# Performance work log

Hardware: AMD Instinct MI355X
Metric: run time of the kernel (lower is better)

The kernel has to match this reference:

```python
import jax, jax.numpy as jnp
import numpy as np

N = 1_000_000
H, W = 480, 640
MIN_DEPTH, MAX_DEPTH = 0.0, 30.0


def setup_inputs() -> dict:
    key = jax.random.key(0)
    k1, k2, k3 = jax.random.split(key, 3)
    scale = jnp.array([W - 1, H - 1], dtype=jnp.float32)
    mkpts0_f = jax.random.uniform(k1, (N, 2), dtype=jnp.float32) * scale
    mkpts1_f = jax.random.uniform(k2, (N, 2), dtype=jnp.float32) * scale
    mconf = jax.random.uniform(k3, (N,), dtype=jnp.float32)
    K = jnp.array([[520.0, 0.0, 320.0],
                   [0.0, 520.0, 240.0],
                   [0.0, 0.0, 1.0]], dtype=jnp.float32)
    K0 = K[None]  # [1,3,3]
    K1 = K[None]
    c, s = float(np.cos(0.1)), float(np.sin(0.1))
    T_0to1 = jnp.array([[c, 0.0, s, 0.2],
                        [0.0, 1.0, 0.0, 0.0],
                        [-s, 0.0, c, 0.05],
                        [0.0, 0.0, 0.0, 1.0]], dtype=jnp.float32)[None]  # [1,4,4]
    image0 = jnp.zeros((1, 1, H, W), dtype=jnp.float32)
    m_bids = jnp.zeros((N,), dtype=jnp.int32)  # single batch element
    return {"T_0to1": T_0to1, "K0": K0, "K1": K1, "mconf": mconf,
            "mkpts0_f": mkpts0_f, "mkpts1_f": mkpts1_f,
            "image0": image0, "m_bids": m_bids}


def _triangulate(T_0to1, K0, K1, mconf, kpts0, kpts1):
    # Projection matrices: P0 = K0 @ [I|0], P1 = K1 @ T[:3,:]
    proj_identity = jnp.eye(3, 4, dtype=K0.dtype)
    P0 = K0[0] @ proj_identity          # [3,4]
    P1 = K1[0] @ T_0to1[0, :3, :]       # [3,4]
    P = jnp.stack([P0, P1], axis=0)     # [V=2,3,4]

    pts = jnp.stack([kpts0, kpts1], axis=1)              # [N,2,2]
    conf = jnp.stack([jnp.ones_like(mconf), mconf], 1)   # [N,2] (self conf = 1)

    # A[n,v] = pts[n,v,:,None] * P[v,2,None,:] - P[v,:2]   -> [N,V,2,4]
    A = pts[..., None] * P[None, :, 2, None, :] - P[None, :, :2, :]
    A = A * conf[:, :, None, None]
    A = A.reshape(A.shape[0], 4, 4)                       # [N,4,4]

    # torch.svd returns V with A = U S V^T; jnp gives Vh = V^T.
    _, _, Vh = jnp.linalg.svd(A)
    v = -Vh[:, 3, :]                                      # [N,4] = -V[:,:,3]
    points_3d = v[:, :3] / v[:, 3:4]                      # homogeneous -> euclidean
    # torch clamps to [-1000,1000] only when infs appear; the final depth value
    # after [0,30] clamp + filter is identical either way, so clip unconditionally.
    points_3d = jnp.clip(points_3d, -1000.0, 1000.0)

    z = jnp.clip(points_3d[:, 2], MIN_DEPTH, MAX_DEPTH)
    filt = (z > MIN_DEPTH) & (z < MAX_DEPTH)
    kp3d_val = z * filt.astype(z.dtype)
    return kp3d_val, points_3d


def reference(T_0to1, K0, K1, mconf, mkpts0_f, mkpts1_f, image0, m_bids):
    h, w = image0.shape[-2], image0.shape[-1]
    kp3d_val, _ = _triangulate(T_0to1, K0, K1, mconf, mkpts0_f, mkpts1_f)
    # generate_sparse_depth: depth[0, y, x] = kp3d_val (long() truncation)
    xi = mkpts0_f[:, 0].astype(jnp.int32)
    yi = mkpts0_f[:, 1].astype(jnp.int32)
    depth0_sparse = jnp.zeros((1, h, w), dtype=kp3d_val.dtype).at[0, yi, xi].set(kp3d_val)
    return depth0_sparse, kp3d_val
```

## Files before the change

kernel.cpp:

```cpp
#include <hip/hip_runtime.h>
#include <math.h>

#define N_PTS 1000000
#define H_IMG 480
#define W_IMG 640
#define PIX (H_IMG * W_IMG)
#define TPB 256
#define BPTS 1024
#define NBLK ((N_PTS + BPTS - 1) / BPTS)


#define ROT64(p, q)                                                            \
  do {                                                                         \
    double apq = Mv[p][q];                                                     \
    if (apq != 0.0) {                                                          \
      double app = Mv[p][p], aqq = Mv[q][q];                                   \
      double d = aqq - app;                                                    \
      double r = sqrt(fma(d, d, 4.0 * apq * apq));                             \
      double t = (2.0 * apq) / (d + copysign(r, d));                           \
      double c = rsqrt(fma(t, t, 1.0));                                        \
      double s = t * c;                                                        \
      Mv[p][p] = fma(-t, apq, app);                                            \
      Mv[q][q] = fma(t, apq, aqq);                                             \
      Mv[p][q] = 0.0;                                                          \
      Mv[q][p] = 0.0;                                                          \
      _Pragma("unroll") for (int k = 0; k < 4; k++) {                          \
        if (k != p && k != q) {                                                \
          double akp = Mv[k][p], akq = Mv[k][q];                               \
          double nkp = c * akp - s * akq;                                      \
          double nkq = s * akp + c * akq;                                      \
          Mv[k][p] = nkp; Mv[p][k] = nkp;                                      \
          Mv[k][q] = nkq; Mv[q][k] = nkq;                                      \
        }                                                                      \
      }                                                                        \
      { double v2p = Vr2[p], v2q = Vr2[q];                                     \
        Vr2[p] = c * v2p - s * v2q; Vr2[q] = s * v2p + c * v2q; }              \
      { double v3p = Vr3[p], v3q = Vr3[q];                                     \
        Vr3[p] = c * v3p - s * v3q; Vr3[q] = s * v3p + c * v3q; }              \
    }                                                                          \
  } while (0)

__device__ float tri_point_fp64(int n,
                                const float* __restrict__ T,
                                const float* __restrict__ K0,
                                const float* __restrict__ K1,
                                const float* __restrict__ mconf,
                                const float* __restrict__ kp0,
                                const float* __restrict__ kp1) {
  float2 p0 = ((const float2*)kp0)[n];
  float2 p1 = ((const float2*)kp1)[n];
  double conf = (double)mconf[n];
  double x0 = (double)p0.x, y0 = (double)p0.y;
  double x1 = (double)p1.x, y1 = (double)p1.y;

  double P0[3][4];
#pragma unroll
  for (int i = 0; i < 3; i++) {
#pragma unroll
    for (int j = 0; j < 3; j++) P0[i][j] = (double)K0[i * 3 + j];
    P0[i][3] = 0.0;
  }
  double P1[3][4];
#pragma unroll
  for (int i = 0; i < 3; i++) {
#pragma unroll
    for (int j = 0; j < 4; j++) {
      double s = 0.0;
#pragma unroll
      for (int k = 0; k < 3; k++)
        s += (double)K1[i * 3 + k] * (double)T[k * 4 + j];
      P1[i][j] = s;
    }
  }

  double Mv[4][4];
#pragma unroll
  for (int i = 0; i < 4; i++)
#pragma unroll
    for (int j = 0; j < 4; j++) Mv[i][j] = 0.0;

  double a[4];
#pragma unroll
  for (int j = 0; j < 4; j++) a[j] = x0 * P0[2][j] - P0[0][j];
#pragma unroll
  for (int i = 0; i < 4; i++)
#pragma unroll
    for (int j = 0; j < 4; j++) Mv[i][j] = fma(a[i], a[j], Mv[i][j]);
#pragma unroll
  for (int j = 0; j < 4; j++) a[j] = y0 * P0[2][j] - P0[1][j];
#pragma unroll
  for (int i = 0; i < 4; i++)
#pragma unroll
    for (int j = 0; j < 4; j++) Mv[i][j] = fma(a[i], a[j], Mv[i][j]);
#pragma unroll
  for (int j = 0; j < 4; j++) a[j] = conf * (x1 * P1[2][j] - P1[0][j]);
#pragma unroll
  for (int i = 0; i < 4; i++)
#pragma unroll
    for (int j = 0; j < 4; j++) Mv[i][j] = fma(a[i], a[j], Mv[i][j]);
#pragma unroll
  for (int j = 0; j < 4; j++) a[j] = conf * (y1 * P1[2][j] - P1[1][j]);
#pragma unroll
  for (int i = 0; i < 4; i++)
#pragma unroll
    for (int j = 0; j < 4; j++) Mv[i][j] = fma(a[i], a[j], Mv[i][j]);

  double Vr2[4] = {0.0, 0.0, 1.0, 0.0};
  double Vr3[4] = {0.0, 0.0, 0.0, 1.0};

  for (int sweep = 0; sweep < 4; sweep++) {
    ROT64(0, 1); ROT64(0, 2); ROT64(0, 3);
    ROT64(1, 2); ROT64(1, 3); ROT64(2, 3);
  }

  double e0 = Mv[0][0], e1 = Mv[1][1], e2 = Mv[2][2], e3 = Mv[3][3];
  bool b01 = e1 < e0;
  double ea = b01 ? e1 : e0;
  double za = b01 ? Vr2[1] : Vr2[0];
  double wa = b01 ? Vr3[1] : Vr3[0];
  bool b23 = e3 < e2;
  double eb = b23 ? e3 : e2;
  double zb = b23 ? Vr2[3] : Vr2[2];
  double wb = b23 ? Vr3[3] : Vr3[2];
  bool bf = eb < ea;
  double vz = bf ? zb : za;
  double vw = bf ? wb : wa;

  double z = vz / vw;
  z = fmin(fmax(z, 0.0), 30.0);
  bool filt = (z > 0.0) && (z < 30.0);
  return filt ? (float)z : 0.0f;
}

#define ROTF(p, q)                                                             \
  do {                                                                         \
    float apq = Mv[p][q];                                                      \
    if (apq != 0.0f) {                                                         \
      float app = Mv[p][p], aqq = Mv[q][q];                                    \
      float d = aqq - app;                                                     \
      float r = sqrtf(fmaf(d, d, 4.0f * apq * apq));                           \
      float t = __fdividef(2.0f * apq, d + copysignf(r, d));                   \
      float c = rsqrtf(fmaf(t, t, 1.0f));                                      \
      float s = t * c;                                                         \
      Mv[p][p] = fmaf(-t, apq, app);                                           \
      Mv[q][q] = fmaf(t, apq, aqq);                                            \
      Mv[p][q] = 0.0f;                                                         \
      Mv[q][p] = 0.0f;                                                         \
      _Pragma("unroll") for (int k = 0; k < 4; k++) {                          \
        if (k != p && k != q) {                                                \
          float akp = Mv[k][p], akq = Mv[k][q];                                \
          float nkp = c * akp - s * akq;                                       \
          float nkq = s * akp + c * akq;                                       \
          Mv[k][p] = nkp; Mv[p][k] = nkp;                                      \
          Mv[k][q] = nkq; Mv[q][k] = nkq;                                      \
        }                                                                      \
      }                                                                        \
      { float v2p = Vr2[p], v2q = Vr2[q];                                      \
        Vr2[p] = c * v2p - s * v2q; Vr2[q] = s * v2p + c * v2q; }              \
      { float v3p = Vr3[p], v3q = Vr3[q];                                      \
        Vr3[p] = c * v3p - s * v3q; Vr3[q] = s * v3p + c * v3q; }              \
    }                                                                          \
  } while (0)

__global__ __launch_bounds__(TPB) void tri_main(
    const float* __restrict__ T,
    const float* __restrict__ K0,
    const float* __restrict__ K1,
    const float* __restrict__ mconf,
    const float* __restrict__ kp0,
    const float* __restrict__ kp1,
    float* __restrict__ out_kp3d,
    unsigned long long* __restrict__ ws_pix)
{
  __shared__ unsigned short s_list[BPTS];
  __shared__ int s_cnt;

  int tid = threadIdx.x;
  int base = blockIdx.x * BPTS;
  if (tid == 0) s_cnt = 0;
  __syncthreads();

  float P0[3][4];
#pragma unroll
  for (int i = 0; i < 3; i++) {
#pragma unroll
    for (int j = 0; j < 3; j++) P0[i][j] = K0[i * 3 + j];
    P0[i][3] = 0.0f;
  }
  float P1[3][4];
#pragma unroll
  for (int i = 0; i < 3; i++) {
#pragma unroll
    for (int j = 0; j < 4; j++) {
      float s = 0.0f;
#pragma unroll
      for (int k = 0; k < 3; k++) s += K1[i * 3 + k] * T[k * 4 + j];
      P1[i][j] = s;
    }
  }

#pragma unroll 1
  for (int r = 0; r < BPTS / TPB; r++) {
    int local = r * TPB + tid;
    int n = base + local;
    if (n >= N_PTS) break;

    float2 p0 = ((const float2*)kp0)[n];
    float2 p1 = ((const float2*)kp1)[n];
    float conf = mconf[n];
    float x0 = p0.x, y0 = p0.y, x1 = p1.x, y1 = p1.y;

    float Mv[4][4];
#pragma unroll
    for (int i = 0; i < 4; i++)
#pragma unroll
      for (int j = 0; j < 4; j++) Mv[i][j] = 0.0f;

    float a[4];
#pragma unroll
    for (int j = 0; j < 4; j++) a[j] = x0 * P0[2][j] - P0[0][j];
#pragma unroll
    for (int i = 0; i < 4; i++)
#pragma unroll
      for (int j = 0; j < 4; j++) Mv[i][j] = fmaf(a[i], a[j], Mv[i][j]);
#pragma unroll
    for (int j = 0; j < 4; j++) a[j] = y0 * P0[2][j] - P0[1][j];
#pragma unroll
    for (int i = 0; i < 4; i++)
#pragma unroll
      for (int j = 0; j < 4; j++) Mv[i][j] = fmaf(a[i], a[j], Mv[i][j]);
#pragma unroll
    for (int j = 0; j < 4; j++) a[j] = conf * (x1 * P1[2][j] - P1[0][j]);
#pragma unroll
    for (int i = 0; i < 4; i++)
#pragma unroll
      for (int j = 0; j < 4; j++) Mv[i][j] = fmaf(a[i], a[j], Mv[i][j]);
#pragma unroll
    for (int j = 0; j < 4; j++) a[j] = conf * (y1 * P1[2][j] - P1[1][j]);
#pragma unroll
    for (int i = 0; i < 4; i++)
#pragma unroll
      for (int j = 0; j < 4; j++) Mv[i][j] = fmaf(a[i], a[j], Mv[i][j]);

    float Vr2[4] = {0.0f, 0.0f, 1.0f, 0.0f};
    float Vr3[4] = {0.0f, 0.0f, 0.0f, 1.0f};

    for (int sweep = 0; sweep < 4; sweep++) {
      ROTF(0, 1); ROTF(0, 2); ROTF(0, 3);
      ROTF(1, 2); ROTF(1, 3); ROTF(2, 3);
    }

    float e0 = Mv[0][0], e1 = Mv[1][1], e2 = Mv[2][2], e3 = Mv[3][3];
    float lo01 = fminf(e0, e1), hi01 = fmaxf(e0, e1);
    float lo23 = fminf(e2, e3), hi23 = fmaxf(e2, e3);
    float emin = fminf(lo01, lo23);
    float esec = fminf(fmaxf(lo01, lo23), fminf(hi01, hi23));
    float trace = e0 + e1 + e2 + e3;

    bool b01 = e1 < e0;
    float za = b01 ? Vr2[1] : Vr2[0];
    float wa = b01 ? Vr3[1] : Vr3[0];
    bool b23 = e3 < e2;
    float zb = b23 ? Vr2[3] : Vr2[2];
    float wb = b23 ? Vr3[3] : Vr3[2];
    bool bf = (b23 ? e3 : e2) < (b01 ? e1 : e0);
    float vz = bf ? zb : za;
    float vw = bf ? wb : wa;

    float z = vz / vw;
    float zc = fminf(fmaxf(z, 0.0f), 30.0f);
    bool filt = (zc > 0.0f) && (zc < 30.0f);
    float kp = filt ? zc : 0.0f;

    float gap = fmaxf(esec - emin, 1e-30f);
    float theta = __fdividef(3e-6f * trace, gap);
    float amp = (1.0f + fminf(fabsf(z), 64.0f)) / fmaxf(fabsf(vw), 1e-6f);
    float err_est = theta * amp;

    bool bad;
    if (!isfinite(z)) {
      bad = true;
    } else if (z > 30.0f) {
      bad = (err_est > z - 30.0f);
    } else {
      bad = (err_est > 30.0f - z) || (err_est > 0.35f && z > -err_est);
    }

    if (!bad) {
      out_kp3d[n] = kp;
      int pix = (int)p0.y * W_IMG + (int)p0.x;
      atomicMax(&ws_pix[pix],
                ((unsigned long long)(0xC0000000u | (unsigned)n) << 32) |
                    (unsigned long long)__float_as_uint(kp));
    } else {
      int idx = atomicAdd(&s_cnt, 1);
      s_list[idx] = (unsigned short)local;
    }
  }

  __syncthreads();

  int cnt = s_cnt;
  for (int i = tid; i < cnt; i += TPB) {
    int n = base + (int)s_list[i];
    float kp = tri_point_fp64(n, T, K0, K1, mconf, kp0, kp1);
    out_kp3d[n] = kp;
    float2 p0 = ((const float2*)kp0)[n];
    int pix = (int)p0.y * W_IMG + (int)p0.x;
    atomicMax(&ws_pix[pix],
              ((unsigned long long)(0xC0000000u | (unsigned)n) << 32) |
                  (unsigned long long)__float_as_uint(kp));
  }
}

__global__ __launch_bounds__(TPB) void unpack_depth(
    const unsigned long long* __restrict__ ws_pix,
    float* __restrict__ out_depth)
{
  int p = blockIdx.x * blockDim.x + threadIdx.x;
  if (p < PIX) {
    unsigned long long v = ws_pix[p];
    unsigned int hi = (unsigned int)(v >> 32);
    out_depth[p] =
        (hi >= 0xC0000000u) ? __uint_as_float((unsigned int)v) : 0.0f;
  }
}

extern "C" void kernel_launch(void* const* d_in, const int* in_sizes, int n_in,
                              void* d_out, int out_size, void* d_ws, size_t ws_size,
                              hipStream_t stream) {
  const float* T     = (const float*)d_in[0];
  const float* K0    = (const float*)d_in[1];
  const float* K1    = (const float*)d_in[2];
  const float* mconf = (const float*)d_in[3];
  const float* kp0   = (const float*)d_in[4];
  const float* kp1   = (const float*)d_in[5];

  float* out = (float*)d_out;
  unsigned long long* ws_pix = (unsigned long long*)d_ws;

  tri_main<<<NBLK, TPB, 0, stream>>>(T, K0, K1, mconf, kp0, kp1,
                                     out + PIX, ws_pix);

  unpack_depth<<<(PIX + TPB - 1) / TPB, TPB, 0, stream>>>(ws_pix, out);
}
```

Baseline: 141.4 us.

## Use fp32 Jacobi for eigenvalues only, recover null vector via fp64 adjugate

The fp32 Jacobi sweeps no longer rotate eigenvector rows; they estimate only the smallest eigenvalues and the spectral gap. The eigenvector is then rebuilt in double precision by forming the normal matrix in fp64, shifting by the smallest eigenvalue, taking the adjugate, and applying it to its dominant column. A new error estimate based on the relative gap decides which points fall back to the full fp64 path. This removes the vector-rotation work from each Jacobi step but adds fp64 arithmetic, which may be slower per operation, and changes which points are flagged for fallback.

```diff
diff --git a/kernel.cpp b/kernel.cpp
--- a/kernel.cpp
+++ b/kernel.cpp
@@ -132,7 +132,7 @@
   return filt ? (float)z : 0.0f;
 }
 
-#define ROTF(p, q)                                                             \
+#define ROTF_NOV(p, q)                                                         \
   do {                                                                         \
     float apq = Mv[p][q];                                                      \
     if (apq != 0.0f) {                                                         \
@@ -143,7 +143,7 @@
       float c = rsqrtf(fmaf(t, t, 1.0f));                                      \
       float s = t * c;                                                         \
       Mv[p][p] = fmaf(-t, apq, app);                                           \
-      Mv[q][q] = fmaf(t, apq, aqq);                                            \
+      Mv[q][q] = fmaf(t, apq, aqq);                                           \
       Mv[p][q] = 0.0f;                                                         \
       Mv[q][p] = 0.0f;                                                         \
       _Pragma("unroll") for (int k = 0; k < 4; k++) {                          \
@@ -155,10 +155,6 @@
           Mv[k][q] = nkq; Mv[q][k] = nkq;                                      \
         }                                                                      \
       }                                                                        \
-      { float v2p = Vr2[p], v2q = Vr2[q];                                      \
-        Vr2[p] = c * v2p - s * v2q; Vr2[q] = s * v2p + c * v2q; }              \
-      { float v3p = Vr3[p], v3q = Vr3[q];                                      \
-        Vr3[p] = c * v3p - s * v3q; Vr3[q] = s * v3p + c * v3q; }              \
     }                                                                          \
   } while (0)
 
@@ -180,22 +176,27 @@
   if (tid == 0) s_cnt = 0;
   __syncthreads();
 
-  float P0[3][4];
+  float P0f[3][4], P1f[3][4];
+  double P0d[3][4], P1d[3][4];
 #pragma unroll
   for (int i = 0; i < 3; i++) {
 #pragma unroll
-    for (int j = 0; j < 3; j++) P0[i][j] = K0[i * 3 + j];
-    P0[i][3] = 0.0f;
-  }
-  float P1[3][4];
+    for (int j = 0; j < 3; j++) {
+      P0f[i][j] = K0[i * 3 + j];
+      P0d[i][j] = (double)K0[i * 3 + j];
+    }
+    P0f[i][3] = 0.0f; P0d[i][3] = 0.0;
+  }
 #pragma unroll
   for (int i = 0; i < 3; i++) {
 #pragma unroll
     for (int j = 0; j < 4; j++) {
-      float s = 0.0f;
-#pragma unroll
-      for (int k = 0; k < 3; k++) s += K1[i * 3 + k] * T[k * 4 + j];
-      P1[i][j] = s;
+      double s = 0.0;
+#pragma unroll
+      for (int k = 0; k < 3; k++)
+        s += (double)K1[i * 3 + k] * (double)T[k * 4 + j];
+      P1d[i][j] = s;
+      P1f[i][j] = (float)s;
     }
   }
 
@@ -207,47 +208,46 @@
 
     float2 p0 = ((const float2*)kp0)[n];
     float2 p1 = ((const float2*)kp1)[n];
-    float conf = mconf[n];
-    float x0 = p0.x, y0 = p0.y, x1 = p1.x, y1 = p1.y;
+    float conff = mconf[n];
 
     float Mv[4][4];
 #pragma unroll
     for (int i = 0; i < 4; i++)
 #pragma unroll
       for (int j = 0; j < 4; j++) Mv[i][j] = 0.0f;
-
-    float a[4];
-#pragma unroll
-    for (int j = 0; j < 4; j++) a[j] = x0 * P0[2][j] - P0[0][j];
-#pragma unroll
-    for (int i = 0; i < 4; i++)
-#pragma unroll
-      for (int j = 0; j < 4; j++) Mv[i][j] = fmaf(a[i], a[j], Mv[i][j]);
-#pragma unroll
-    for (int j = 0; j < 4; j++) a[j] = y0 * P0[2][j] - P0[1][j];
-#pragma unroll
-    for (int i = 0; i < 4; i++)
-#pragma unroll
-      for (int j = 0; j < 4; j++) Mv[i][j] = fmaf(a[i], a[j], Mv[i][j]);
-#pragma unroll
-    for (int j = 0; j < 4; j++) a[j] = conf * (x1 * P1[2][j] - P1[0][j]);
-#pragma unroll
-    for (int i = 0; i < 4; i++)
-#pragma unroll
-      for (int j = 0; j < 4; j++) Mv[i][j] = fmaf(a[i], a[j], Mv[i][j]);
-#pragma unroll
-    for (int j = 0; j < 4; j++) a[j] = conf * (y1 * P1[2][j] - P1[1][j]);
-#pragma unroll
-    for (int i = 0; i < 4; i++)
-#pragma unroll
-      for (int j = 0; j < 4; j++) Mv[i][j] = fmaf(a[i], a[j], Mv[i][j]);
-
-    float Vr2[4] = {0.0f, 0.0f, 1.0f, 0.0f};
-    float Vr3[4] = {0.0f, 0.0f, 0.0f, 1.0f};
+    {
+      float af[4];
+#pragma unroll
+      for (int j = 0; j < 4; j++) af[j] = p0.x * P0f[2][j] - P0f[0][j];
+#pragma unroll
+      for (int i = 0; i < 4; i++)
+#pragma unroll
+        for (int j = 0; j < 4; j++) Mv[i][j] = fmaf(af[i], af[j], Mv[i][j]);
+#pragma unroll
+      for (int j = 0; j < 4; j++) af[j] = p0.y * P0f[2][j] - P0f[1][j];
+#pragma unroll
+      for (int i = 0; i < 4; i++)
+#pragma unroll
+        for (int j = 0; j < 4; j++) Mv[i][j] = fmaf(af[i], af[j], Mv[i][j]);
+#pragma unroll
+      for (int j = 0; j < 4; j++)
+        af[j] = conff * (p1.x * P1f[2][j] - P1f[0][j]);
+#pragma unroll
+      for (int i = 0; i < 4; i++)
+#pragma unroll
+        for (int j = 0; j < 4; j++) Mv[i][j] = fmaf(af[i], af[j], Mv[i][j]);
+#pragma unroll
+      for (int j = 0; j < 4; j++)
+        af[j] = conff * (p1.y * P1f[2][j] - P1f[1][j]);
+#pragma unroll
+      for (int i = 0; i < 4; i++)
+#pragma unroll
+        for (int j = 0; j < 4; j++) Mv[i][j] = fmaf(af[i], af[j], Mv[i][j]);
+    }
 
     for (int sweep = 0; sweep < 4; sweep++) {
-      ROTF(0, 1); ROTF(0, 2); ROTF(0, 3);
-      ROTF(1, 2); ROTF(1, 3); ROTF(2, 3);
+      ROTF_NOV(0, 1); ROTF_NOV(0, 2); ROTF_NOV(0, 3);
+      ROTF_NOV(1, 2); ROTF_NOV(1, 3); ROTF_NOV(2, 3);
     }
 
     float e0 = Mv[0][0], e1 = Mv[1][1], e2 = Mv[2][2], e3 = Mv[3][3];
@@ -256,37 +256,103 @@
     float emin = fminf(lo01, lo23);
     float esec = fminf(fmaxf(lo01, lo23), fminf(hi01, hi23));
     float trace = e0 + e1 + e2 + e3;
-
-    bool b01 = e1 < e0;
-    float za = b01 ? Vr2[1] : Vr2[0];
-    float wa = b01 ? Vr3[1] : Vr3[0];
-    bool b23 = e3 < e2;
-    float zb = b23 ? Vr2[3] : Vr2[2];
-    float wb = b23 ? Vr3[3] : Vr3[2];
-    bool bf = (b23 ? e3 : e2) < (b01 ? e1 : e0);
-    float vz = bf ? zb : za;
-    float vw = bf ? wb : wa;
-
-    float z = vz / vw;
-    float zc = fminf(fmaxf(z, 0.0f), 30.0f);
-    bool filt = (zc > 0.0f) && (zc < 30.0f);
-    float kp = filt ? zc : 0.0f;
-
-    float gap = fmaxf(esec - emin, 1e-30f);
-    float theta = __fdividef(3e-6f * trace, gap);
-    float amp = (1.0f + fminf(fabsf(z), 64.0f)) / fmaxf(fabsf(vw), 1e-6f);
-    float err_est = theta * amp;
-
-    bool bad;
-    if (!isfinite(z)) {
-      bad = true;
-    } else if (z > 30.0f) {
-      bad = (err_est > z - 30.0f);
-    } else {
-      bad = (err_est > 30.0f - z) || (err_est > 0.35f && z > -err_est);
-    }
+    float g = (esec - emin) / fmaxf(trace, 1e-30f);
+
+    double m00, m01, m02, m03, m11, m12, m13, m22, m23, m33;
+    m00 = m01 = m02 = m03 = m11 = m12 = m13 = m22 = m23 = m33 = 0.0;
+    {
+      double x0 = (double)p0.x, y0 = (double)p0.y;
+      double x1 = (double)p1.x, y1 = (double)p1.y;
+      double cf = (double)conff;
+      double a[4];
+#pragma unroll
+      for (int rr = 0; rr < 4; rr++) {
+        if (rr == 0) {
+#pragma unroll
+          for (int j = 0; j < 4; j++) a[j] = fma(x0, P0d[2][j], -P0d[0][j]);
+        } else if (rr == 1) {
+#pragma unroll
+          for (int j = 0; j < 4; j++) a[j] = fma(y0, P0d[2][j], -P0d[1][j]);
+        } else if (rr == 2) {
+#pragma unroll
+          for (int j = 0; j < 4; j++)
+            a[j] = cf * fma(x1, P1d[2][j], -P1d[0][j]);
+        } else {
+#pragma unroll
+          for (int j = 0; j < 4; j++)
+            a[j] = cf * fma(y1, P1d[2][j], -P1d[1][j]);
+        }
+        m00 = fma(a[0], a[0], m00); m01 = fma(a[0], a[1], m01);
+        m02 = fma(a[0], a[2], m02); m03 = fma(a[0], a[3], m03);
+        m11 = fma(a[1], a[1], m11); m12 = fma(a[1], a[2], m12);
+        m13 = fma(a[1], a[3], m13); m22 = fma(a[2], a[2], m22);
+        m23 = fma(a[2], a[3], m23); m33 = fma(a[3], a[3], m33);
+      }
+    }
+
+    double mu = (double)emin;
+    double b00 = m00 - mu, b11 = m11 - mu, b22 = m22 - mu, b33 = m33 - mu;
+    double b01 = m01, b02 = m02, b03 = m03, b12 = m12, b13 = m13, b23 = m23;
+
+    double s0 = fma(b00, b11, -b01 * b01);
+    double s1 = fma(b00, b12, -b02 * b01);
+    double s2 = fma(b00, b13, -b03 * b01);
+    double s3 = fma(b01, b12, -b02 * b11);
+    double s4 = fma(b01, b13, -b03 * b11);
+    double c0 = fma(b02, b13, -b12 * b03);
+    double c1 = fma(b02, b23, -b22 * b03);
+    double c2 = fma(b02, b33, -b23 * b03);
+    double c3 = fma(b12, b23, -b22 * b13);
+    double c4 = fma(b12, b33, -b23 * b13);
+    double c5 = fma(b22, b33, -b23 * b23);
+
+    double a00 = fma(b11, c5, fma(-b12, c4, b13 * c3));
+    double a01 = -fma(b01, c5, fma(-b02, c4, b03 * c3));
+    double a11 = fma(b00, c5, fma(-b02, c2, b03 * c1));
+    double a02 = fma(b01, c4, fma(-b11, c2, b13 * c0));
+    double a12 = -fma(b00, c4, fma(-b01, c2, b03 * c0));
+    double a22 = fma(b03, s4, fma(-b13, s2, b33 * s0));
+    double a03 = -fma(b01, c3, fma(-b11, c1, b12 * c0));
+    double a13 = fma(b00, c3, fma(-b01, c1, b02 * c0));
+    double a23 = -fma(b03, s3, fma(-b13, s1, b23 * s0));
+    double a33 = fma(b02, s3, fma(-b12, s1, b22 * s0));
+
+    double w10 = a00, w11 = a01, w12 = a02, w13 = a03;
+    double bd = fabs(a00);
+    { double d1 = fabs(a11);
+      bool c = d1 > bd;
+      w10 = c ? a01 : w10; w11 = c ? a11 : w11;
+      w12 = c ? a12 : w12; w13 = c ? a13 : w13; bd = c ? d1 : bd; }
+    { double d2 = fabs(a22);
+      bool c = d2 > bd;
+      w10 = c ? a02 : w10; w11 = c ? a12 : w11;
+      w12 = c ? a22 : w12; w13 = c ? a23 : w13; bd = c ? d2 : bd; }
+    { double d3 = fabs(a33);
+      bool c = d3 > bd;
+      w10 = c ? a03 : w10; w11 = c ? a13 : w11;
+      w12 = c ? a23 : w12; w13 = c ? a33 : w13; }
+
+    double w0 = fma(a00, w10, fma(a01, w11, fma(a02, w12, a03 * w13)));
+    double w1 = fma(a01, w10, fma(a11, w11, fma(a12, w12, a13 * w13)));
+    double w2 = fma(a02, w10, fma(a12, w11, fma(a22, w12, a23 * w13)));
+    double w3 = fma(a03, w10, fma(a13, w11, fma(a23, w12, a33 * w13)));
+
+    double inv3 = 1.0 / w3;
+    double z = w2 * inv3;
+
+    double wn = fmax(fmax(fabs(w0), fabs(w1)), fmax(fabs(w2), fabs(w3)));
+    double gd = (double)fmaxf(g, 1e-30f);
+    double theta = 5e-13 / (gd * gd);
+    double err_z = theta * wn * (fabs(w2) + fabs(w3)) * (inv3 * inv3);
+    err_z = fabs(err_z);
+
+    bool bad = (g < 1e-5f) || !isfinite(z) ||
+               (err_z > 0.3) || (fabs(z - 30.0) < err_z);
 
     if (!bad) {
+      double zc = fmin(fmax(z, 0.0), 30.0);
+      bool filt = (zc > 0.0) && (zc < 30.0);
+      float kp = filt ? (float)zc : 0.0f;
       out_kp3d[n] = kp;
       int pix = (int)p0.y * W_IMG + (int)p0.x;
       atomicMax(&ws_pix[pix],
```

Result: no change. 139.8 us (-1.1%).
